# Optimization experiments

Hardware: AMD Instinct MI355X
Metric: run time of the kernel (lower is better)

Reference implementation:

```python
import jax, jax.numpy as jnp
import numpy as np

IMG_H, IMG_W = 256, 704  # full image shape (img_metas['img_shape'])
EPS = 1e-5
B, N_CAM, D_REF, C_CH = 1, 6, 1, 256
HF, WF = 32, 88
DD = 64
BEV_H = BEV_W = 128
Q = BEV_H * BEV_W


def inverse_sigmoid(x, eps=1e-5):
    x = jnp.clip(x, 0.0, 1.0)
    return jnp.log(jnp.clip(x, eps) / jnp.clip(1.0 - x, eps))


def grid_sample_2d(feat, grid):
    # feat [N,C,H,W], grid [N,Hg,Wg,2] (x,y in [-1,1]); bilinear, zeros padding, align_corners=False
    Nn, C, H, W = feat.shape
    x = (grid[..., 0] + 1.0) * 0.5 * W - 0.5
    y = (grid[..., 1] + 1.0) * 0.5 * H - 0.5
    x0 = jnp.floor(x)
    y0 = jnp.floor(y)
    wx = x - x0
    wy = y - y0
    x0 = x0.astype(jnp.int32)
    y0 = y0.astype(jnp.int32)

    def gather(ix, iy):
        valid = (ix >= 0) & (ix < W) & (iy >= 0) & (iy < H)
        ixc = jnp.clip(ix, 0, W - 1)
        iyc = jnp.clip(iy, 0, H - 1)
        v = jax.vmap(lambda f, jx, jy: f[:, jy, jx])(feat, ixc, iyc)  # [N,C,Hg,Wg]
        return v * valid[:, None].astype(feat.dtype)

    return (gather(x0, y0) * ((1 - wx) * (1 - wy))[:, None]
            + gather(x0 + 1, y0) * (wx * (1 - wy))[:, None]
            + gather(x0, y0 + 1) * ((1 - wx) * wy)[:, None]
            + gather(x0 + 1, y0 + 1) * (wx * wy)[:, None])


def grid_sample_3d(vol, grid):
    # vol [N,C,D,H,W], grid [N,Dg,Hg,Wg,3] (x,y,z); trilinear, zeros padding, align_corners=False
    Nn, C, D, H, W = vol.shape
    x = (grid[..., 0] + 1.0) * 0.5 * W - 0.5
    y = (grid[..., 1] + 1.0) * 0.5 * H - 0.5
    z = (grid[..., 2] + 1.0) * 0.5 * D - 0.5
    x0 = jnp.floor(x); y0 = jnp.floor(y); z0 = jnp.floor(z)
    wx = x - x0; wy = y - y0; wz = z - z0
    x0 = x0.astype(jnp.int32); y0 = y0.astype(jnp.int32); z0 = z0.astype(jnp.int32)

    def gather(ix, iy, iz):
        valid = (ix >= 0) & (ix < W) & (iy >= 0) & (iy < H) & (iz >= 0) & (iz < D)
        ixc = jnp.clip(ix, 0, W - 1)
        iyc = jnp.clip(iy, 0, H - 1)
        izc = jnp.clip(iz, 0, D - 1)
        v = jax.vmap(lambda f, jx, jy, jz: f[:, jz, jy, jx])(vol, ixc, iyc, izc)
        return v * valid[:, None].astype(vol.dtype)

    return (gather(x0, y0, z0) * ((1 - wx) * (1 - wy) * (1 - wz))[:, None]
            + gather(x0 + 1, y0, z0) * (wx * (1 - wy) * (1 - wz))[:, None]
            + gather(x0, y0 + 1, z0) * ((1 - wx) * wy * (1 - wz))[:, None]
            + gather(x0 + 1, y0 + 1, z0) * (wx * wy * (1 - wz))[:, None]
            + gather(x0, y0, z0 + 1) * ((1 - wx) * (1 - wy) * wz)[:, None]
            + gather(x0 + 1, y0, z0 + 1) * (wx * (1 - wy) * wz)[:, None]
            + gather(x0, y0 + 1, z0 + 1) * ((1 - wx) * wy * wz)[:, None]
            + gather(x0 + 1, y0 + 1, z0 + 1) * (wx * wy * wz)[:, None])


def setup_inputs() -> dict:
    key = jax.random.key(0)
    ks = jax.random.split(key, 12)
    feat = jax.random.normal(ks[0], (B * N_CAM, C_CH, HF, WF), jnp.float32)
    bev_queries = jax.random.normal(ks[1], (B, Q, C_CH), jnp.float32)
    bev_pos = jax.random.normal(ks[2], (B, Q, C_CH), jnp.float32)
    reference_points = jax.random.uniform(ks[3], (B, D_REF, Q, 3), jnp.float32)
    pc_range = jnp.array([-51.2, -51.2, -5.0, 51.2, 51.2, 3.0], jnp.float32)
    # semi-realistic lidar->image projection matrices: intrinsics * axis-swap * yaw per camera
    f, cx, cy = 500.0, IMG_W / 2.0, IMG_H / 2.0
    K = np.array([[f, 0, cx, 0], [0, f, cy, 0], [0, 0, 1, 0], [0, 0, 0, 1]], np.float32)
    A = np.array([[0, -1, 0, 0], [0, 0, -1, 0], [1, 0, 0, 0], [0, 0, 0, 1]], np.float32)
    mats = []
    for i in range(N_CAM):
        th = 2.0 * np.pi * i / N_CAM
        c, s = np.cos(th), np.sin(th)
        R = np.array([[c, s, 0, 0], [-s, c, 0, 0], [0, 0, 1, 0], [0, 0, 0, 1]], np.float32)
        mats.append(K @ A @ R)
    lidar_to_img = jnp.asarray(np.stack(mats))[None]  # [1,N,4,4]
    depth_prob = jax.random.uniform(ks[4], (B * N_CAM, DD, HF, WF), jnp.float32)
    sc = 0.02
    return {
        'feat': feat, 'bev_queries': bev_queries, 'bev_pos': bev_pos,
        'reference_points': reference_points, 'pc_range': pc_range,
        'lidar_to_img': lidar_to_img, 'depth_prob': depth_prob,
        'w_pos': jax.random.normal(ks[5], (C_CH, 1), jnp.float32) * sc,
        'b_pos': jnp.zeros((1,), jnp.float32),
        'w_img': jax.random.normal(ks[6], (C_CH, N_CAM * 2), jnp.float32) * sc,
        'b_img': jnp.zeros((N_CAM * 2,), jnp.float32),
        'w_att': jax.random.normal(ks[7], (C_CH, N_CAM), jnp.float32) * sc,
        'b_att': jnp.zeros((N_CAM,), jnp.float32),
        'conv_w': jax.random.normal(ks[8], (C_CH, C_CH, 3, 3), jnp.float32) * sc,
        'conv_b': jnp.zeros((C_CH,), jnp.float32),
        'bn_gamma': jnp.ones((C_CH,), jnp.float32),
        'bn_beta': jnp.zeros((C_CH,), jnp.float32),
        'bn_mean': jnp.zeros((C_CH,), jnp.float32),
        'bn_var': jnp.ones((C_CH,), jnp.float32),
        'se_w': jax.random.normal(ks[9], (C_CH, C_CH), jnp.float32) * sc,
        'se_b': jnp.zeros((C_CH,), jnp.float32),
        'cbam_w': jax.random.normal(ks[10], (1, 2, 7, 7), jnp.float32) * 0.05,
        'cbam_b': jnp.zeros((1,), jnp.float32),
        'bev_h': BEV_H, 'bev_w': BEV_W,
    }


def reference(feat, bev_queries, bev_pos, reference_points, pc_range, lidar_to_img, depth_prob,
              w_pos, b_pos, w_img, b_img, w_att, b_att, conv_w, conv_b,
              bn_gamma, bn_beta, bn_mean, bn_var, se_w, se_b, cbam_w, cbam_b, bev_h, bev_w):
    Bq, Qn = bev_queries.shape[:2]
    D = reference_points.shape[1]
    N = lidar_to_img.shape[1]
    BN, C, Hf, Wf = feat.shape
    q = bev_queries + bev_pos
    pos_offset = q @ w_pos + b_pos  # [B,Q,1] (only_use_height)
    z = jax.nn.sigmoid(inverse_sigmoid(reference_points[..., 2:3]) + pos_offset[:, None])
    rp = jnp.concatenate([reference_points[..., :2], z], axis=-1)  # [B,D,Q,3]
    attn = (q @ w_att + b_att).reshape(Bq, 1, Qn, N, 1)
    img_off = q @ w_img + b_img  # [B,Q,2N]
    # unnormalize to lidar coords; apply_3d_transformation == identity (no aug)
    pts = rp * (pc_range[3:] - pc_range[:3]) + pc_range[:3]
    pts4 = jnp.concatenate([pts, jnp.ones_like(pts[..., :1])], axis=-1)  # [B,D,Q,4]
    cam = jnp.einsum('bnij,bdqj->dbnqi', lidar_to_img, pts4)  # [D,B,N,Q,4]
    ref_depth = cam[..., 2:3]
    mask = ref_depth > EPS
    xy = cam[..., :2] / jnp.maximum(cam[..., 2:3], EPS)
    xy = xy / jnp.array([IMG_W, IMG_H], dtype=xy.dtype)
    xy = (xy - 0.5) * 2.0
    mask = mask & (xy[..., 0:1] > -1.0) & (xy[..., 0:1] < 1.0) & (xy[..., 1:2] > -1.0) & (xy[..., 1:2] < 1.0)
    Dd = depth_prob.shape[1]
    ref_depth = (ref_depth / Dd - 0.5) * 2.0
    mask = mask & (ref_depth > -1.0) & (ref_depth < 1.0)
    bev_mask = jnp.transpose(mask, (1, 4, 3, 2, 0)).astype(feat.dtype)  # [B,1,Q,N,D]
    off = img_off.reshape(Bq, Qn, N, 2).transpose(0, 2, 1, 3)[None] / jnp.array([Wf, Hf], dtype=feat.dtype)
    xy = xy + off  # [D,B,N,Q,2]
    grid = xy.transpose(1, 2, 3, 0, 4).reshape(BN, Qn, D, 2)
    sampled = grid_sample_2d(feat, grid).reshape(Bq, N, C, Qn, D).transpose(0, 2, 3, 1, 4)  # [B,C,Q,N,D]
    grid3 = jnp.concatenate([xy, ref_depth], axis=-1).transpose(1, 2, 3, 0, 4).reshape(BN, 1, Qn, D, 3)
    dp = grid_sample_3d(depth_prob[:, None], grid3).reshape(Bq, N, 1, Qn, D).transpose(0, 2, 3, 1, 4)
    bev_mask = jnp.nan_to_num(dp) * bev_mask
    w = jax.nn.sigmoid(attn) * jnp.nan_to_num(bev_mask)
    agg = (jnp.nan_to_num(sampled) * w)[..., 0].sum(-1)  # [B,C,Q] (D==1)
    x = agg.reshape(Bq, C, bev_h, bev_w)
    dn = ('NCHW', 'OIHW', 'NCHW')
    x = jax.lax.conv_general_dilated(x, conv_w, (1, 1), ((1, 1), (1, 1)), dimension_numbers=dn) + conv_b[None, :, None, None]
    x = (x - bn_mean[None, :, None, None]) * (bn_gamma / jnp.sqrt(bn_var + 1e-5))[None, :, None, None] + bn_beta[None, :, None, None]
    x = jax.nn.relu(x)
    s = x.mean(axis=(2, 3))  # SE: global avg pool + 1x1 conv + sigmoid
    x = x * jax.nn.sigmoid(s @ se_w.T + se_b)[:, :, None, None]
    a = jnp.concatenate([x.max(axis=1, keepdims=True), x.mean(axis=1, keepdims=True)], axis=1)  # CBAM spatial
    a = jax.lax.conv_general_dilated(a, cbam_w, (1, 1), ((3, 3), (3, 3)), dimension_numbers=dn) + cbam_b[None, :, None, None]
    x = x * jax.nn.sigmoid(a)
    out = x.reshape(Bq, C, bev_h * bev_w).transpose(0, 2, 1)
    return out, rp
```

## Files before the change

kernel.cpp:

```cpp
#include <hip/hip_runtime.h>
#include <math.h>

#define QN   16384
#define CCH  256
#define NCAM 6
#define HFD  32
#define WFD  88
#define DDD  64
#define BEVH 128
#define BEVW 128
#define IMGW 704.0f
#define IMGH 256.0f
#define EPSV 1e-5f

typedef __attribute__((ext_vector_type(8))) short bf8_t;
typedef __attribute__((ext_vector_type(8))) unsigned short us8;
typedef __attribute__((ext_vector_type(4))) unsigned short us4;
typedef __attribute__((ext_vector_type(4))) float f4_t;

__device__ __forceinline__ float sigmoidf_(float x){ return 1.0f/(1.0f+__expf(-x)); }

__device__ __forceinline__ unsigned short f2bf(float f){
    unsigned int b = __float_as_uint(f);
    b += 0x7FFFu + ((b >> 16) & 1u);
    return (unsigned short)(b >> 16);
}
__device__ __forceinline__ float bf2f(unsigned short u){
    return __uint_as_float(((unsigned int)u) << 16);
}

__global__ __launch_bounds__(256) void k_prep(const float* __restrict__ feat, unsigned short* __restrict__ feat_tH,
                                              const float* __restrict__ cw, unsigned short* __restrict__ wtH,
                                              const float* __restrict__ se_w, float* __restrict__ se_wT,
                                              float* __restrict__ ssum){
    int b = blockIdx.x;
    if (b < 4224){
        __shared__ float tile[32][33];
        int n   = b / 704;
        int rem = b - n*704;
        int cb  = (rem / 88) * 32;
        int pb  = (rem % 88) * 32;
        int tx = threadIdx.x & 31, ty = threadIdx.x >> 5;
        for (int r = ty; r < 32; r += 8)
            tile[r][tx] = feat[(size_t)(n*256 + cb + r)*2816 + pb + tx];
        __syncthreads();
        for (int r = ty; r < 32; r += 8)
            feat_tH[(size_t)(n*2816 + pb + r)*256 + cb + tx] = f2bf(tile[tx][r]);
    } else if (b < 6528){
        int b2 = b - 4224;
        if (b2 == 0) ssum[threadIdx.x] = 0.f;
        int idx = b2*256 + threadIdx.x;
        int ci = idx & 255;
        int co = (idx >> 8) & 255;
        int kk = idx >> 16;
        int kh = kk/3, kw = kk - kh*3;
        int chunk = ci >> 6, ciin = ci & 63;
        size_t dst = ((((size_t)(kh*4 + chunk)*3 + kw)*256 + co) << 6) + ciin;
        wtH[dst] = f2bf(cw[(size_t)(co*256 + ci)*9 + kk]);
    } else {
        __shared__ float tile[32][33];
        int tb = b - 6528;
        int rb_ = (tb >> 3) * 32;
        int cb_ = (tb & 7) * 32;
        int tx = threadIdx.x & 31, ty = threadIdx.x >> 5;
        for (int r = ty; r < 32; r += 8)
            tile[r][tx] = se_w[(size_t)(rb_ + r)*256 + cb_ + tx];
        __syncthreads();
        for (int r = ty; r < 32; r += 8)
            se_wT[(size_t)(cb_ + r)*256 + rb_ + tx] = tile[tx][r];
    }
}

__global__ __launch_bounds__(256) void k_geomagg(
    const float* __restrict__ bq, const float* __restrict__ bpos,
    const float* __restrict__ refp, const float* __restrict__ pcr,
    const float* __restrict__ l2i, const float* __restrict__ dpr,
    const float* __restrict__ w_pos, const float* __restrict__ b_pos,
    const float* __restrict__ w_img, const float* __restrict__ b_img,
    const float* __restrict__ w_att, const float* __restrict__ b_att,
    const unsigned short* __restrict__ feat_tH,
    unsigned short* __restrict__ aggH, float* __restrict__ out_rp)
{
    __shared__ float wl[19][256];
    __shared__ float sprj[8][24];
    __shared__ int   so_l[192];
    __shared__ float sw_l[192];
    int q0 = blockIdx.x * 8;
    int tid = threadIdx.x;
    int wid = tid >> 6, lane = tid & 63;
    int c0 = lane * 4;

    wl[0][tid] = w_pos[tid];
    #pragma unroll
    for (int r = 0; r < 6; r++){
        int idx = r*256 + tid;
        int c = idx / 6, j = idx - 6*c;
        wl[1 + j][c] = w_att[idx];
    }
    #pragma unroll
    for (int r = 0; r < 12; r++){
        int idx = r*256 + tid;
        int c = idx / 12, j = idx - 12*c;
        wl[7 + j][c] = w_img[idx];
    }
    __syncthreads();

    #pragma unroll
    for (int qi = 0; qi < 2; qi++){
        int ql = wid*2 + qi;
        int q  = q0 + ql;

        const float4 a4 = *(const float4*)(bq  + (size_t)q*CCH + c0);
        const float4 b4 = *(const float4*)(bpos+ (size_t)q*CCH + c0);
        float qv[4] = {a4.x+b4.x, a4.y+b4.y, a4.z+b4.z, a4.w+b4.w};

        float s[19];
        #pragma unroll
        for (int j = 0; j < 19; j++){
            const float4 wv = *(const float4*)&wl[j][c0];
            s[j] = qv[0]*wv.x + qv[1]*wv.y + qv[2]*wv.z + qv[3]*wv.w;
        }
        #pragma unroll
        for (int off=1; off<64; off<<=1){
            #pragma unroll
            for (int i=0;i<19;i++) s[i] += __shfl_xor(s[i], off, 64);
        }

        if (lane == 0){
            float pos_off = s[0] + b_pos[0];
            float rx = refp[q*3+0], ry = refp[q*3+1], rz = refp[q*3+2];
            float zc_ = fminf(fmaxf(rz, 0.f), 1.f);
            float inv = logf(fmaxf(zc_, EPSV) / fmaxf(1.f - zc_, EPSV));
            float znew = sigmoidf_(inv + pos_off);
            out_rp[q*3+0] = rx; out_rp[q*3+1] = ry; out_rp[q*3+2] = znew;
            #pragma unroll
            for (int j=0;j<19;j++) sprj[ql][j] = s[j];
            sprj[ql][19] = znew; sprj[ql][20] = rx; sprj[ql][21] = ry;
        }
    }
    __syncthreads();

    {
        int sub = lane >> 5;
        int n   = lane & 31;
        if (n < NCAM){
            int ql = wid*2 + sub;
            float att  = sprj[ql][1+n] + b_att[n];
            float offx = (sprj[ql][7+2*n] + b_img[2*n])   / (float)WFD;
            float offy = (sprj[ql][8+2*n] + b_img[2*n+1]) / (float)HFD;
            float znew = sprj[ql][19], rx = sprj[ql][20], ry = sprj[ql][21];
            float lo0=pcr[0], lo1=pcr[1], lo2=pcr[2];
            float hi0=pcr[3], hi1=pcr[4], hi2=pcr[5];
            float px = rx*(hi0-lo0)+lo0, py = ry*(hi1-lo1)+lo1, pz = znew*(hi2-lo2)+lo2;
            const float* M = l2i + n*16;
            float cx = M[0]*px + M[1]*py + M[2]*pz  + M[3];
            float cy = M[4]*px + M[5]*py + M[6]*pz  + M[7];
            float cz = M[8]*px + M[9]*py + M[10]*pz + M[11];
            bool m = cz > EPSV;
            float zdiv = fmaxf(cz, EPSV);
            float u = (cx/zdiv)/IMGW; u = (u - 0.5f)*2.f;
            float v = (cy/zdiv)/IMGH; v = (v - 0.5f)*2.f;
            m = m && (u > -1.f) && (u < 1.f) && (v > -1.f) && (v < 1.f);
            float rdn = (cz/(float)DDD - 0.5f)*2.f;
            m = m && (rdn > -1.f) && (rdn < 1.f);

            int base = ql*24 + n*4;
            float wq = 0.f, xs = 0.f, ys = 0.f;
            if (m){
                float u2 = u + offx, v2 = v + offy;
                xs = (u2 + 1.f)*0.5f*WFD - 0.5f;
                ys = (v2 + 1.f)*0.5f*HFD - 0.5f;
                float zs = (rdn + 1.f)*0.5f*DDD - 0.5f;
                float fx = floorf(xs), fy = floorf(ys), fz = floorf(zs);
                int x0=(int)fx, y0=(int)fy, z0=(int)fz;
                float wx = xs-fx, wy = ys-fy, wz = zs-fz;
                float dp = 0.f;
                const float* vol = dpr + (size_t)n*DDD*HFD*WFD;
                #pragma unroll
                for (int dz=0; dz<2; dz++)
                #pragma unroll
                for (int dy=0; dy<2; dy++)
                #pragma unroll
                for (int dx=0; dx<2; dx++){
                    int ix=x0+dx, iy=y0+dy, iz=z0+dz;
                    if (ix>=0 && ix<WFD && iy>=0 && iy<HFD && iz>=0 && iz<DDD){
                        float ww = (dx?wx:1.f-wx)*(dy?wy:1.f-wy)*(dz?wz:1.f-wz);
                        dp += ww * vol[(size_t)(iz*HFD+iy)*WFD + ix];
                    }
                }
                wq = sigmoidf_(att) * dp;
            }
            if (m && wq != 0.f){
                float fx = floorf(xs), fy = floorf(ys);
                int x0=(int)fx, y0=(int)fy;
                float wx = xs-fx, wy = ys-fy;
                float cwv[4] = {(1.f-wx)*(1.f-wy), wx*(1.f-wy), (1.f-wx)*wy, wx*wy};
                int xi[4] = {x0, x0+1, x0, x0+1};
                int yi[4] = {y0, y0, y0+1, y0+1};
                #pragma unroll
                for (int k=0;k<4;k++){
                    bool ok = (xi[k]>=0 && xi[k]<WFD && yi[k]>=0 && yi[k]<HFD);
                    so_l[base+k] = ok ? ((n*HFD + yi[k])*WFD + xi[k]) : 0;
                    sw_l[base+k] = ok ? wq*cwv[k] : 0.f;
                }
            } else {
                #pragma unroll
                for (int k=0;k<4;k++){ so_l[base+k] = 0; sw_l[base+k] = 0.f; }
            }
        }
    }
    __syncthreads();

    {
        int half = lane >> 5, li = lane & 31;
        int c8 = li * 8;
        int ql = wid*2 + half;
        float a[8] = {0.f,0.f,0.f,0.f,0.f,0.f,0.f,0.f};
        #pragma unroll
        for (int k=0;k<24;k++){
            float w = sw_l[ql*24+k];
            if (w != 0.f){
                us8 v = *(const us8*)(feat_tH + (size_t)so_l[ql*24+k]*CCH + c8);
                #pragma unroll
                for (int j=0;j<8;j++) a[j] += w * bf2f((unsigned short)v[j]);
            }
        }
        us8 o;
        #pragma unroll
        for (int j=0;j<8;j++) o[j] = f2bf(a[j]);
        *(us8*)(aggH + (size_t)(q0+ql)*CCH + c8) = o;
    }
}

__global__ __launch_bounds__(256, 2) void k_conv2(const unsigned short* __restrict__ aggH,
    const unsigned short* __restrict__ wtH, const float* __restrict__ conv_b,
    const float* __restrict__ bn_g, const float* __restrict__ bn_b,
    const float* __restrict__ bn_m, const float* __restrict__ bn_v,
    float* __restrict__ xN, float* __restrict__ ssum)
{
    __shared__ unsigned short Al[130][72];
    __shared__ unsigned short Bl[3][128][72];
    __shared__ float sacc[128];

    int h   = blockIdx.x;
    int co0 = blockIdx.y * 128;
    int tid  = threadIdx.x;
    int lane = tid & 63, wid = tid >> 6;
    int m_q = (wid & 1) * 64;
    int n_q = (wid >> 1) * 64;
    int l15 = lane & 15, quad = lane >> 4;

    f4_t acc[4][4];
    #pragma unroll
    for (int i=0;i<4;i++)
    #pragma unroll
    for (int j=0;j<4;j++) acc[i][j] = (f4_t){0.f,0.f,0.f,0.f};

    int arow = tid >> 1;
    int aseg = (tid & 1) * 32;

    if (tid < 16){
        int r = (tid >> 3) ? 129 : 0;
        int sg = (tid & 7) * 8;
        *(us8*)&Al[r][sg] = (us8){0,0,0,0,0,0,0,0};
    }
    if (tid < 128) sacc[tid] = 0.f;

    us8 ra[4], rb[3][4];
    const us8 z8 = (us8){0,0,0,0,0,0,0,0};

    #define LOADSTAGE(s) { \
        int kh_ = (s) >> 2; int ci0_ = ((s) & 3) << 6; \
        int ph_ = h + kh_ - 1; \
        if (ph_ >= 0 && ph_ < BEVH){ \
            const unsigned short* ap_ = aggH + ((size_t)(ph_*BEVW + arow)*CCH + ci0_ + aseg); \
            ra[0] = *(const us8*)ap_;      ra[1] = *(const us8*)(ap_ + 8); \
            ra[2] = *(const us8*)(ap_ + 16); ra[3] = *(const us8*)(ap_ + 24); \
        } else { ra[0]=z8; ra[1]=z8; ra[2]=z8; ra[3]=z8; } \
        const unsigned short* bp_ = wtH + (size_t)(s)*49152 + (size_t)co0*64; \
        _Pragma("unroll") \
        for (int kw_=0; kw_<3; kw_++){ \
            _Pragma("unroll") \
            for (int j_=0; j_<4; j_++) \
                rb[kw_][j_] = *(const us8*)(bp_ + kw_*16384 + (j_*256 + tid)*8); \
        } \
    }

    LOADSTAGE(0);
    for (int s=0; s<12; s++){
        __syncthreads();
        *(us8*)&Al[arow+1][aseg]      = ra[0];
        *(us8*)&Al[arow+1][aseg+8]    = ra[1];
        *(us8*)&Al[arow+1][aseg+16]   = ra[2];
        *(us8*)&Al[arow+1][aseg+24]   = ra[3];
        {
            int bco = tid >> 3;
            int ciin = (tid & 7) * 8;
            #pragma unroll
            for (int kw_=0; kw_<3; kw_++){
                #pragma unroll
                for (int j_=0; j_<4; j_++)
                    *(us8*)&Bl[kw_][j_*32 + bco][ciin] = rb[kw_][j_];
            }
        }
        __syncthreads();
        if (s < 11) LOADSTAGE(s+1);
        #pragma unroll
        for (int ks=0; ks<2; ks++){
            #pragma unroll
            for (int kw=0; kw<3; kw++){
                bf8_t af[4], bfr[4];
                #pragma unroll
                for (int i=0;i<4;i++) af[i]  = *(bf8_t*)&Al[m_q + i*16 + l15 + kw][ks*32 + quad*8];
                #pragma unroll
                for (int j=0;j<4;j++) bfr[j] = *(bf8_t*)&Bl[kw][n_q + j*16 + l15][ks*32 + quad*8];
                #pragma unroll
                for (int i=0;i<4;i++)
                #pragma unroll
                for (int j=0;j<4;j++)
                    acc[i][j] = __builtin_amdgcn_mfma_f32_16x16x32_bf16(af[i], bfr[j], acc[i][j], 0, 0, 0);
            }
        }
    }
    #undef LOADSTAGE

    #pragma unroll
    for (int j=0;j<4;j++){
        int col = n_q + j*16 + l15;
        int co = co0 + col;
        float sc = bn_g[co] * rsqrtf(bn_v[co] + 1e-5f);
        float sh = bn_b[co] - bn_m[co]*sc;
        float cb = conv_b[co];
        float part = 0.f;
        #pragma unroll
        for (int i=0;i<4;i++){
            #pragma unroll
            for (int r=0;r<4;r++){
                int m = m_q + i*16 + quad*4 + r;
                int p = h*BEVW + m;
                float y = fmaxf((acc[i][j][r] + cb)*sc + sh, 0.f);
                xN[(size_t)p*CCH + co] = y;
                part += y;
            }
        }
        atomicAdd(&sacc[col], part);
    }
    __syncthreads();
    if (tid < 128) atomicAdd(&ssum[co0 + tid], sacc[tid]);
}

__global__ __launch_bounds__(256) void k_maps2(const float* __restrict__ xN,
    const float* __restrict__ ssum, const float* __restrict__ se_wT, const float* __restrict__ se_b,
    float* __restrict__ scale_g, float* __restrict__ amax, float* __restrict__ amean)
{
    __shared__ float smv[256];
    __shared__ float scl[256];
    int t = threadIdx.x;
    smv[t] = ssum[t] * (1.f/16384.f);
    __syncthreads();
    float a0=0.f, a1=0.f, a2=0.f, a3=0.f;
    for (int k=0; k<256; k+=4){
        a0 += smv[k]   * se_wT[(size_t)(k  )*256 + t];
        a1 += smv[k+1] * se_wT[(size_t)(k+1)*256 + t];
        a2 += smv[k+2] * se_wT[(size_t)(k+2)*256 + t];
        a3 += smv[k+3] * se_wT[(size_t)(k+3)*256 + t];
    }
    float sv = sigmoidf_(se_b[t] + ((a0+a1)+(a2+a3)));
    scl[t] = sv;
    if (blockIdx.x == 0) scale_g[t] = sv;
    __syncthreads();

    int wid = t >> 6, lane = t & 63;
    int p0 = blockIdx.x * 64;
    float4 sc = *(const float4*)&scl[lane*4];
    for (int i=0; i<16; i++){
        int p = p0 + i*4 + wid;
        float4 v = *(const float4*)&xN[(size_t)p*CCH + lane*4];
        float a = v.x*sc.x, b = v.y*sc.y, c = v.z*sc.z, d = v.w*sc.w;
        float mx = fmaxf(fmaxf(a,b), fmaxf(c,d));
        float sm = a+b+c+d;
        #pragma unroll
        for (int off=1; off<64; off<<=1){
            mx = fmaxf(mx, __shfl_xor(mx, off, 64));
            sm += __shfl_xor(sm, off, 64);
        }
        if (lane == 0){ amax[p] = mx; amean[p] = sm*(1.f/256.f); }
    }
}

__global__ __launch_bounds__(256) void k_final2(const float* __restrict__ xN,
    const float* __restrict__ scale_g, const float* __restrict__ amax, const float* __restrict__ amean,
    const float* __restrict__ cw, const float* __restrict__ cb, float* __restrict__ out)
{
    __shared__ float am2[7][128];
    __shared__ float av2[7][128];
    __shared__ float wcb[98];
    __shared__ float scl[256];
    __shared__ float amap_l[64];

    int b = blockIdx.x;
    int h  = b >> 1;
    int w0 = (b & 1) * 64;
    int t = threadIdx.x;

    scl[t] = scale_g[t];
    if (t < 98) wcb[t] = cw[t];
    for (int idx = t; idx < 896; idx += 256){
        int r = idx >> 7, c = idx & 127;
        int ph = h + r - 3;
        bool ok = (ph >= 0 && ph < BEVH);
        am2[r][c] = ok ? amax[ph*BEVW + c] : 0.f;
        av2[r][c] = ok ? amean[ph*BEVW + c] : 0.f;
    }
    __syncthreads();

    if (t < 64){
        int px = w0 + t;
        float acc = cb[0];
        #pragma unroll
        for (int kh=0; kh<7; kh++){
            #pragma unroll
            for (int kw=0; kw<7; kw++){
                int pw = px + kw - 3;
                if (pw >= 0 && pw < BEVW)
                    acc += am2[kh][pw]*wcb[kh*7+kw] + av2[kh][pw]*wcb[49 + kh*7+kw];
            }
        }
        amap_l[t] = sigmoidf_(acc);
    }
    __syncthreads();

    int lane = t & 63, sub = t >> 6;
    int c4 = lane * 4;
    float4 sc = *(const float4*)&scl[c4];
    for (int i=0; i<16; i++){
        int pxl = sub*16 + i;
        int p = h*BEVW + w0 + pxl;
        float am = amap_l[pxl];
        float4 v = *(const float4*)&xN[(size_t)p*CCH + c4];
        float4 o;
        o.x = v.x*sc.x*am; o.y = v.y*sc.y*am; o.z = v.z*sc.z*am; o.w = v.w*sc.w*am;
        *(float4*)&out[(size_t)p*CCH + c4] = o;
    }
}

extern "C" void kernel_launch(void* const* d_in, const int* in_sizes, int n_in,
                              void* d_out, int out_size, void* d_ws, size_t ws_size,
                              hipStream_t stream) {
    const float* feat   = (const float*)d_in[0];
    const float* bq     = (const float*)d_in[1];
    const float* bpos   = (const float*)d_in[2];
    const float* refp   = (const float*)d_in[3];
    const float* pcr    = (const float*)d_in[4];
    const float* l2i    = (const float*)d_in[5];
    const float* dpr    = (const float*)d_in[6];
    const float* w_pos  = (const float*)d_in[7];
    const float* b_pos  = (const float*)d_in[8];
    const float* w_img  = (const float*)d_in[9];
    const float* b_img  = (const float*)d_in[10];
    const float* w_att  = (const float*)d_in[11];
    const float* b_att  = (const float*)d_in[12];
    const float* conv_w = (const float*)d_in[13];
    const float* conv_b = (const float*)d_in[14];
    const float* bn_g   = (const float*)d_in[15];
    const float* bn_b   = (const float*)d_in[16];
    const float* bn_m   = (const float*)d_in[17];
    const float* bn_v   = (const float*)d_in[18];
    const float* se_w   = (const float*)d_in[19];
    const float* se_b   = (const float*)d_in[20];
    const float* cbw    = (const float*)d_in[21];
    const float* cbb    = (const float*)d_in[22];
    float* out = (float*)d_out;

    float* ws = (float*)d_ws;
    size_t o = 0;
    unsigned short* feat_tH = (unsigned short*)(ws + o); o += (size_t)6*2816*128;
    unsigned short* wtH  = (unsigned short*)(ws + o); o += (size_t)9*256*128;
    unsigned short* aggH = (unsigned short*)(ws + o); o += (size_t)QN*128;
    float* xN      = ws + o;  o += (size_t)QN*256;
    float* se_wT   = ws + o;  o += (size_t)256*256;
    float* ssum    = ws + o;  o += 256;
    float* scale_g = ws + o;  o += 256;
    float* amax    = ws + o;  o += QN;
    float* amean   = ws + o;  o += QN;

    k_prep<<<6592, 256, 0, stream>>>(feat, feat_tH, conv_w, wtH, se_w, se_wT, ssum);
    k_geomagg<<<2048, 256, 0, stream>>>(bq, bpos, refp, pcr, l2i, dpr,
                                        w_pos, b_pos, w_img, b_img, w_att, b_att,
                                        feat_tH, aggH, out + (size_t)QN*256);
    k_conv2<<<dim3(128,2), 256, 0, stream>>>(aggH, wtH, conv_b, bn_g, bn_b, bn_m, bn_v, xN, ssum);
    k_maps2<<<256, 256, 0, stream>>>(xN, ssum, se_wT, se_b, scale_g, amax, amean);
    k_final2<<<256, 256, 0, stream>>>(xN, scale_g, amax, amean, cbw, cbb, out);
}
```

Before: 238.5 us.

## Split query projection into separate MFMA kernel and drop zero-weight gather branch

Moves the 256-to-19 query projection out of the gather kernel into a new kernel that runs it as bf16 MFMA matmuls over 64-query tiles and writes the 19 projections plus the new z to a global scratch buffer. The gather kernel then reads those values instead of doing per-wave shuffle reductions and reloading the weight matrix into shared memory in every block. The zero-weight branch in the feature gather is also removed so all 24 samples are loaded unconditionally. This adds a kernel launch and a scratch round-trip, computes the projection in bf16 instead of fp32, and may read feature rows for masked samples that were skipped before.

```diff
diff --git a/kernel.cpp b/kernel.cpp
--- a/kernel.cpp
+++ b/kernel.cpp
@@ -71,73 +71,110 @@
     }
 }
 
+__global__ __launch_bounds__(256) void k_proj(
+    const float* __restrict__ bq, const float* __restrict__ bpos,
+    const float* __restrict__ refp,
+    const float* __restrict__ w_pos, const float* __restrict__ b_pos,
+    const float* __restrict__ w_img, const float* __restrict__ w_att,
+    float* __restrict__ Sg, float* __restrict__ out_rp)
+{
+    __shared__ float wlf[19][260];
+    __shared__ unsigned short Aq[64][264];
+    __shared__ float sl[64][20];
+    int tid = threadIdx.x;
+    int lane = tid & 63, wid = tid >> 6;
+    int l15 = lane & 15, quad = lane >> 4;
+    int q0 = blockIdx.x * 64;
+
+    wlf[0][tid] = w_pos[tid];
+    #pragma unroll
+    for (int r = 0; r < 6; r++){
+        int idx = r*256 + tid;
+        int c = idx / 6, j = idx - 6*c;
+        wlf[1 + j][c] = w_att[idx];
+    }
+    #pragma unroll
+    for (int r = 0; r < 12; r++){
+        int idx = r*256 + tid;
+        int c = idx / 12, j = idx - 12*c;
+        wlf[7 + j][c] = w_img[idx];
+    }
+    #pragma unroll
+    for (int r = 0; r < 16; r++){
+        int row = r*4 + wid;
+        int cc  = lane * 4;
+        float4 a = *(const float4*)(bq   + (size_t)(q0+row)*CCH + cc);
+        float4 b = *(const float4*)(bpos + (size_t)(q0+row)*CCH + cc);
+        us4 o;
+        o.x = f2bf(a.x+b.x); o.y = f2bf(a.y+b.y); o.z = f2bf(a.z+b.z); o.w = f2bf(a.w+b.w);
+        *(us4*)&Aq[row][cc] = o;
+    }
+    __syncthreads();
+
+    f4_t acc0 = (f4_t){0.f,0.f,0.f,0.f};
+    f4_t acc1 = (f4_t){0.f,0.f,0.f,0.f};
+    #pragma unroll
+    for (int kc = 0; kc < 8; kc++){
+        bf8_t af = *(bf8_t*)&Aq[wid*16 + l15][kc*32 + quad*8];
+        bf8_t b0, b1;
+        {
+            const float* wr = &wlf[l15][kc*32 + quad*8];
+            float4 w0 = *(const float4*)wr;
+            float4 w1 = *(const float4*)(wr + 4);
+            b0[0]=(short)f2bf(w0.x); b0[1]=(short)f2bf(w0.y); b0[2]=(short)f2bf(w0.z); b0[3]=(short)f2bf(w0.w);
+            b0[4]=(short)f2bf(w1.x); b0[5]=(short)f2bf(w1.y); b0[6]=(short)f2bf(w1.z); b0[7]=(short)f2bf(w1.w);
+        }
+        if (l15 < 3){
+            const float* wr = &wlf[16 + l15][kc*32 + quad*8];
+            float4 w0 = *(const float4*)wr;
+            float4 w1 = *(const float4*)(wr + 4);
+            b1[0]=(short)f2bf(w0.x); b1[1]=(short)f2bf(w0.y); b1[2]=(short)f2bf(w0.z); b1[3]=(short)f2bf(w0.w);
+            b1[4]=(short)f2bf(w1.x); b1[5]=(short)f2bf(w1.y); b1[6]=(short)f2bf(w1.z); b1[7]=(short)f2bf(w1.w);
+        } else {
+            b1 = (bf8_t){0,0,0,0,0,0,0,0};
+        }
+        acc0 = __builtin_amdgcn_mfma_f32_16x16x32_bf16(af, b0, acc0, 0, 0, 0);
+        acc1 = __builtin_amdgcn_mfma_f32_16x16x32_bf16(af, b1, acc1, 0, 0, 0);
+    }
+    #pragma unroll
+    for (int r = 0; r < 4; r++){
+        int qq = wid*16 + quad*4 + r;
+        sl[qq][l15] = acc0[r];
+        if (l15 < 3) sl[qq][16 + l15] = acc1[r];
+    }
+    __syncthreads();
+
+    if (tid < 64){
+        int q = q0 + tid;
+        float pos_off = sl[tid][0] + b_pos[0];
+        float rx = refp[q*3+0], ry = refp[q*3+1], rz = refp[q*3+2];
+        float zc_ = fminf(fmaxf(rz, 0.f), 1.f);
+        float inv = logf(fmaxf(zc_, EPSV) / fmaxf(1.f - zc_, EPSV));
+        float znew = sigmoidf_(inv + pos_off);
+        out_rp[q*3+0] = rx; out_rp[q*3+1] = ry; out_rp[q*3+2] = znew;
+        sl[tid][19] = znew;
+    }
+    __syncthreads();
+
+    for (int i = tid; i < 64*20; i += 256)
+        Sg[(size_t)q0*20 + i] = ((const float*)sl)[i];
+}
+
 __global__ __launch_bounds__(256) void k_geomagg(
-    const float* __restrict__ bq, const float* __restrict__ bpos,
     const float* __restrict__ refp, const float* __restrict__ pcr,
     const float* __restrict__ l2i, const float* __restrict__ dpr,
-    const float* __restrict__ w_pos, const float* __restrict__ b_pos,
-    const float* __restrict__ w_img, const float* __restrict__ b_img,
-    const float* __restrict__ w_att, const float* __restrict__ b_att,
-    const unsigned short* __restrict__ feat_tH,
-    unsigned short* __restrict__ aggH, float* __restrict__ out_rp)
+    const float* __restrict__ b_img, const float* __restrict__ b_att,
+    const float* __restrict__ Sg, const unsigned short* __restrict__ feat_tH,
+    unsigned short* __restrict__ aggH)
 {
-    __shared__ float wl[19][256];
-    __shared__ float sprj[8][24];
+    __shared__ float sgl[8][20];
     __shared__ int   so_l[192];
     __shared__ float sw_l[192];
     int q0 = blockIdx.x * 8;
     int tid = threadIdx.x;
     int wid = tid >> 6, lane = tid & 63;
-    int c0 = lane * 4;
-
-    wl[0][tid] = w_pos[tid];
-    #pragma unroll
-    for (int r = 0; r < 6; r++){
-        int idx = r*256 + tid;
-        int c = idx / 6, j = idx - 6*c;
-        wl[1 + j][c] = w_att[idx];
-    }
-    #pragma unroll
-    for (int r = 0; r < 12; r++){
-        int idx = r*256 + tid;
-        int c = idx / 12, j = idx - 12*c;
-        wl[7 + j][c] = w_img[idx];
-    }
-    __syncthreads();
-
-    #pragma unroll
-    for (int qi = 0; qi < 2; qi++){
-        int ql = wid*2 + qi;
-        int q  = q0 + ql;
-
-        const float4 a4 = *(const float4*)(bq  + (size_t)q*CCH + c0);
-        const float4 b4 = *(const float4*)(bpos+ (size_t)q*CCH + c0);
-        float qv[4] = {a4.x+b4.x, a4.y+b4.y, a4.z+b4.z, a4.w+b4.w};
-
-        float s[19];
-        #pragma unroll
-        for (int j = 0; j < 19; j++){
-            const float4 wv = *(const float4*)&wl[j][c0];
-            s[j] = qv[0]*wv.x + qv[1]*wv.y + qv[2]*wv.z + qv[3]*wv.w;
-        }
-        #pragma unroll
-        for (int off=1; off<64; off<<=1){
-            #pragma unroll
-            for (int i=0;i<19;i++) s[i] += __shfl_xor(s[i], off, 64);
-        }
-
-        if (lane == 0){
-            float pos_off = s[0] + b_pos[0];
-            float rx = refp[q*3+0], ry = refp[q*3+1], rz = refp[q*3+2];
-            float zc_ = fminf(fmaxf(rz, 0.f), 1.f);
-            float inv = logf(fmaxf(zc_, EPSV) / fmaxf(1.f - zc_, EPSV));
-            float znew = sigmoidf_(inv + pos_off);
-            out_rp[q*3+0] = rx; out_rp[q*3+1] = ry; out_rp[q*3+2] = znew;
-            #pragma unroll
-            for (int j=0;j<19;j++) sprj[ql][j] = s[j];
-            sprj[ql][19] = znew; sprj[ql][20] = rx; sprj[ql][21] = ry;
-        }
-    }
+
+    if (tid < 160) ((float*)sgl)[tid] = Sg[(size_t)q0*20 + tid];
     __syncthreads();
 
     {
@@ -145,10 +182,12 @@
         int n   = lane & 31;
         if (n < NCAM){
             int ql = wid*2 + sub;
-            float att  = sprj[ql][1+n] + b_att[n];
-            float offx = (sprj[ql][7+2*n] + b_img[2*n])   / (float)WFD;
-            float offy = (sprj[ql][8+2*n] + b_img[2*n+1]) / (float)HFD;
-            float znew = sprj[ql][19], rx = sprj[ql][20], ry = sprj[ql][21];
+            int q  = q0 + ql;
+            float att  = sgl[ql][1+n] + b_att[n];
+            float offx = (sgl[ql][7+2*n] + b_img[2*n])   / (float)WFD;
+            float offy = (sgl[ql][8+2*n] + b_img[2*n+1]) / (float)HFD;
+            float znew = sgl[ql][19];
+            float rx = refp[q*3+0], ry = refp[q*3+1];
             float lo0=pcr[0], lo1=pcr[1], lo2=pcr[2];
             float hi0=pcr[3], hi1=pcr[4], hi2=pcr[5];
             float px = rx*(hi0-lo0)+lo0, py = ry*(hi1-lo1)+lo1, pz = znew*(hi2-lo2)+lo2;
@@ -219,11 +258,9 @@
         #pragma unroll
         for (int k=0;k<24;k++){
             float w = sw_l[ql*24+k];
-            if (w != 0.f){
-                us8 v = *(const us8*)(feat_tH + (size_t)so_l[ql*24+k]*CCH + c8);
-                #pragma unroll
-                for (int j=0;j<8;j++) a[j] += w * bf2f((unsigned short)v[j]);
-            }
+            us8 v = *(const us8*)(feat_tH + (size_t)so_l[ql*24+k]*CCH + c8);
+            #pragma unroll
+            for (int j=0;j<8;j++) a[j] += w * bf2f((unsigned short)v[j]);
         }
         us8 o;
         #pragma unroll
@@ -270,11 +307,11 @@
     const us8 z8 = (us8){0,0,0,0,0,0,0,0};
 
     #define LOADSTAGE(s) { \
-        int kh_ = (s) >> 2; int ci0_ = ((s) & 3) << 6; \
+        int kh_ = (s) >> 2; \
         int ph_ = h + kh_ - 1; \
         if (ph_ >= 0 && ph_ < BEVH){ \
-            const unsigned short* ap_ = aggH + ((size_t)(ph_*BEVW + arow)*CCH + ci0_ + aseg); \
-            ra[0] = *(const us8*)ap_;      ra[1] = *(const us8*)(ap_ + 8); \
+            const unsigned short* ap_ = aggH + ((size_t)(ph_*BEVW + arow)*CCH + (((s) & 3) << 6) + aseg); \
+            ra[0] = *(const us8*)ap_;        ra[1] = *(const us8*)(ap_ + 8); \
             ra[2] = *(const us8*)(ap_ + 16); ra[3] = *(const us8*)(ap_ + 24); \
         } else { ra[0]=z8; ra[1]=z8; ra[2]=z8; ra[3]=z8; } \
         const unsigned short* bp_ = wtH + (size_t)(s)*49152 + (size_t)co0*64; \
@@ -479,15 +516,17 @@
     unsigned short* aggH = (unsigned short*)(ws + o); o += (size_t)QN*128;
     float* xN      = ws + o;  o += (size_t)QN*256;
     float* se_wT   = ws + o;  o += (size_t)256*256;
+    float* Sg      = ws + o;  o += (size_t)QN*20;
     float* ssum    = ws + o;  o += 256;
     float* scale_g = ws + o;  o += 256;
     float* amax    = ws + o;  o += QN;
     float* amean   = ws + o;  o += QN;
 
     k_prep<<<6592, 256, 0, stream>>>(feat, feat_tH, conv_w, wtH, se_w, se_wT, ssum);
-    k_geomagg<<<2048, 256, 0, stream>>>(bq, bpos, refp, pcr, l2i, dpr,
-                                        w_pos, b_pos, w_img, b_img, w_att, b_att,
-                                        feat_tH, aggH, out + (size_t)QN*256);
+    k_proj<<<256, 256, 0, stream>>>(bq, bpos, refp, w_pos, b_pos, w_img, w_att,
+                                    Sg, out + (size_t)QN*256);
+    k_geomagg<<<2048, 256, 0, stream>>>(refp, pcr, l2i, dpr, b_img, b_att,
+                                        Sg, feat_tH, aggH);
     k_conv2<<<dim3(128,2), 256, 0, stream>>>(aggH, wtH, conv_b, bn_g, bn_b, bn_m, bn_v, xN, ssum);
     k_maps2<<<256, 256, 0, stream>>>(xN, ssum, se_wT, se_b, scale_g, amax, amean);
     k_final2<<<256, 256, 0, stream>>>(xN, scale_g, amax, amean, cbw, cbb, out);
```

Result: faster. 221.9 us (-7.0%).
